# Optimization experiments

Hardware: AMD Instinct MI355X
Metric: run time of the kernel (lower is better)

The kernel has to match this reference:

```python
import jax, jax.numpy as jnp
import numpy as np

B, T, D = 4, 2048, 1024
HEADS = 8
D_K = D // HEADS


def setup_inputs() -> dict:
    key = jax.random.key(0)
    kq, kk, kv = jax.random.split(key, 3)
    return {
        "query": jax.random.normal(kq, (B, T, D), dtype=jnp.float32),
        "key": jax.random.normal(kk, (B, T, D), dtype=jnp.float32),
        "value": jax.random.normal(kv, (B, T, D), dtype=jnp.float32),
    }


def reference(query, key, value):
    b, t, d = query.shape
    # [B,T,D] -> [B,H,T,d_k]
    q = query.reshape(b, t, HEADS, D_K).transpose(0, 2, 1, 3)
    k = key.reshape(b, t, HEADS, D_K).transpose(0, 2, 1, 3)
    v = value.reshape(b, t, HEADS, D_K).transpose(0, 2, 1, 3)
    scale = 1.0 / jnp.sqrt(jnp.asarray(D_K, dtype=q.dtype))
    scores = jnp.einsum("bhqd,bhkd->bhqk", q, k) * scale  # [B,H,T,T]
    p_attn = jax.nn.softmax(scores, axis=-1)
    # sharpening: second softmax over 1000*p, clamp to [0,1]
    attn = jnp.clip(jax.nn.softmax(1000.0 * p_attn, axis=-1), 0.0, 1.0)
    x = jnp.einsum("bhqk,bhkd->bhqd", attn, v)  # [B,H,T,d_k]
    out = x.transpose(0, 2, 1, 3).reshape(b, t, HEADS * D_K)
    return out
```

## Files before the change

### kernel.cpp

```cpp
#include <hip/hip_runtime.h>


typedef __attribute__((ext_vector_type(4))) float f32x4;
typedef __attribute__((ext_vector_type(16))) float f32x16;
typedef __attribute__((ext_vector_type(8))) _Float16 h16x8;
typedef __attribute__((ext_vector_type(4))) _Float16 h16x4;
typedef __attribute__((ext_vector_type(8))) short s16x8;
typedef __attribute__((ext_vector_type(4))) short s16x4;
typedef __attribute__((ext_vector_type(2))) unsigned int u32x2;
typedef __attribute__((ext_vector_type(4))) unsigned int u32x4;

#define NB 4
#define T_ 2048
#define D_ 1024
#define NH 8
#define DK 128
#define BQ 64
#define NWG (NB * NH * (T_ / BQ))
#define KB2 32
#define NKC2 (T_ / KB2)
#define SCALE 0.08838834764831845f
#define SC2   0.12751741689839996f
#define MOFF2 11.541560327111707f
#define L2E   1.4426950408889634f

__device__ __forceinline__ unsigned int pk2(float a, float b) {
  return __builtin_bit_cast(unsigned int, __builtin_amdgcn_cvt_pkrtz(a, b));
}
#define H8(p) __builtin_bit_cast(h16x8, *(const s16x8*)(p))

__device__ __forceinline__ void gload16(const unsigned short* g, unsigned short* l) {
  __builtin_amdgcn_global_load_lds(
      (const __attribute__((address_space(1))) void*)g,
      (__attribute__((address_space(3))) void*)l, 16, 0, 0);
}

__global__ __launch_bounds__(256) void cvtK16(const float* __restrict__ Kg,
                                              unsigned short* __restrict__ K16) {
  const int t = threadIdx.x;
#pragma unroll
  for (int i = 0; i < 4; ++i) {
    const unsigned gid = blockIdx.x * 1024u + i * 256u + t;
    const unsigned bhk = gid >> 4, dg = gid & 15u;
    const unsigned b = bhk >> 14, rem = bhk & 16383u;
    const unsigned h = rem >> 11, k = rem & 2047u;
    const float* s = Kg + ((size_t)b * T_ + k) * D_ + h * DK + dg * 8;
    f32x4 x0 = *(const f32x4*)s, x1 = *(const f32x4*)(s + 4);
    h16x8 hv;
#pragma unroll
    for (int j = 0; j < 4; ++j) { hv[j] = (_Float16)x0[j]; hv[j + 4] = (_Float16)x1[j]; }
    *(u32x4*)(K16 + (size_t)gid * 8) = __builtin_bit_cast(u32x4, hv);
  }
}

__global__ __launch_bounds__(256) void trV16(const float* __restrict__ Vg,
                                             unsigned short* __restrict__ V16t) {
  __shared__ float vt[64][129];
  const int t = threadIdx.x;
  const int bh = blockIdx.x >> 5;
  const int kc = blockIdx.x & 31;
  const int b = bh >> 3, h = bh & 7;
  const float* src = Vg + ((size_t)b * T_ + kc * 64) * D_ + h * DK;
#pragma unroll
  for (int p = 0; p < 8; ++p) {
    const int j = t + p * 256;
    const int row = j >> 5, c4 = j & 31;
    f32x4 v = *(const f32x4*)(src + (size_t)row * D_ + c4 * 4);
#pragma unroll
    for (int i = 0; i < 4; ++i) vt[row][c4 * 4 + i] = v[i];
  }
  __syncthreads();
  unsigned short* dst = V16t + (size_t)bh * DK * T_ + (size_t)kc * 64;
#pragma unroll
  for (int i = 0; i < 4; ++i) {
    const int gg = t + i * 256;
    const int d = gg >> 3, kg = gg & 7;
    u32x4 pv;
#pragma unroll
    for (int jj = 0; jj < 4; ++jj)
      pv[jj] = pk2(vt[kg * 8 + 2 * jj][d], vt[kg * 8 + 2 * jj + 1][d]);
    *(u32x4*)(dst + (size_t)d * T_ + kg * 8) = pv;
  }
}

__global__ __launch_bounds__(128, 2) void simattn_v8(
    const float* __restrict__ Qg, const unsigned short* __restrict__ K16,
    const unsigned short* __restrict__ V16t, float* __restrict__ Og) {
  __shared__ __align__(16) unsigned short kf[2][KB2 * DK];
  __shared__ __align__(16) unsigned short vts[2][DK * KB2];

  const int tid  = threadIdx.x;
  const int wid2 = tid >> 6;
  const int lane = tid & 63;
  const int c    = lane & 31;
  const int g    = lane >> 5;
  const bool hi  = (g != 0);

  const int blk  = (blockIdx.x & 7) * (NWG >> 3) + (blockIdx.x >> 3);
  const int qblk = blk & (T_ / BQ - 1);
  const int h    = (blk >> 5) & (NH - 1);
  const int b    = blk >> 8;
  const int q0   = qblk * BQ;
  const size_t bh  = (size_t)b * (T_ * D_) + (size_t)h * DK;
  const int    bhp = b * NH + h;
  const unsigned short* kp16 = K16 + (size_t)bhp * (T_ * DK);
  const unsigned short* vp16 = V16t + (size_t)bhp * (DK * T_);

  h16x8 qf[8];
  {
    const float* qp = Qg + bh + (size_t)(q0 + wid2 * 32 + c) * D_;
#pragma unroll
    for (int step = 0; step < 8; ++step) {
      const int d0 = step * 16 + g * 8;
      f32x4 x0 = *(const f32x4*)(qp + d0);
      f32x4 x1 = *(const f32x4*)(qp + d0 + 4);
#pragma unroll
      for (int i = 0; i < 4; ++i) {
        qf[step][i]     = (_Float16)x0[i];
        qf[step][i + 4] = (_Float16)x1[i];
      }
    }
  }

  int koffs[4], voffs[4], ldst[4];
#pragma unroll
  for (int i = 0; i < 4; ++i) {
    const int id = wid2 * 4 + i;
    ldst[i] = id * 512 + lane * 8;
    {
      const int r = id * 4 + (lane >> 4), t = lane & 15;
      const int sk = 4 * ((id >> 1) & 1);
      koffs[i] = r * DK + ((((t - sk) & 15) ^ (r & 7)) * 8);
    }
    {
      const int d = id * 16 + (lane >> 2), t = lane & 3;
      voffs[i] = d * T_ + ((t ^ ((d >> 1) & 3)) * 8);
    }
  }
  auto stK = [&](int kc, int buf) {
    const unsigned short* s0 = kp16 + (size_t)kc * (KB2 * DK);
#pragma unroll
    for (int i = 0; i < 4; ++i) gload16(s0 + koffs[i], &kf[buf][ldst[i]]);
  };
  auto stV = [&](int kc, int buf) {
    const unsigned short* s0 = vp16 + kc * KB2;
#pragma unroll
    for (int i = 0; i < 4; ++i) gload16(s0 + voffs[i], &vts[buf][ldst[i]]);
  };

  int kread[8];
  {
    const int xr = c & 7, skr = 4 * ((c >> 3) & 1);
#pragma unroll
    for (int step = 0; step < 8; ++step)
      kread[step] = c * DK + (((((2 * step + g) ^ xr) + skr) & 15) * 8);
  }
  const int vsw = (c >> 1) & 3;

  auto qkT = [&](int buf) {
    f32x16 st;
#pragma unroll
    for (int i = 0; i < 16; ++i) st[i] = 0.f;
#pragma unroll
    for (int step = 0; step < 8; ++step) {
      st = __builtin_amdgcn_mfma_f32_32x32x16_f16(H8(&kf[buf][kread[step]]),
                                                  qf[step], st, 0, 0, 0);
    }
    return st;
  };

  float msc = -3.0e38f, l8 = 0.f;
  stK(0, 0);
  __syncthreads();
  for (int kc = 0; kc < NKC2; ++kc) {
    if (kc + 1 < NKC2) stK(kc + 1, (kc + 1) & 1);
    f32x16 st = qkT(kc & 1);
    float e[16];
#pragma unroll
    for (int r = 0; r < 16; ++r) {
      msc = fmaxf(msc, st[r]);
      e[r] = __builtin_amdgcn_exp2f(fmaf(st[r], SC2, -MOFF2));
    }
    float s0 = 0.f, s1 = 0.f, s2 = 0.f, s3 = 0.f;
#pragma unroll
    for (int r = 0; r < 4; ++r) {
      s0 += e[r]; s1 += e[4 + r]; s2 += e[8 + r]; s3 += e[12 + r];
    }
    l8 += (s0 + s1) + (s2 + s3);
    __syncthreads();
  }
  msc = fmaxf(msc, __shfl_xor(msc, 32));
  l8 += __shfl_xor(l8, 32);
  const float pm   = __builtin_amdgcn_exp2f(fmaf(msc, SC2, -MOFF2));
  const float ul2  = (1000.0f / l8) * L2E;
  const float mcu2 = -ul2 * pm;

  f32x16 y[4];
#pragma unroll
  for (int dt = 0; dt < 4; ++dt)
#pragma unroll
    for (int i = 0; i < 16; ++i) y[dt][i] = 0.f;
  float Wl = 0.f;

  stK(0, 0);
  stV(0, 0);
  __syncthreads();
  for (int kc = 0; kc < NKC2; ++kc) {
    if (kc + 1 < NKC2) { stK(kc + 1, (kc + 1) & 1); stV(kc + 1, (kc + 1) & 1); }
    const int buf = kc & 1;
    f32x16 st = qkT(buf);

    unsigned pw[8];
#pragma unroll
    for (int m = 0; m < 8; ++m) {
      const float p0 = __builtin_amdgcn_exp2f(fmaf(st[2 * m], SC2, -MOFF2));
      const float p1 = __builtin_amdgcn_exp2f(fmaf(st[2 * m + 1], SC2, -MOFF2));
      const float w0 = __builtin_amdgcn_exp2f(fmaf(p0, ul2, mcu2));
      const float w1 = __builtin_amdgcn_exp2f(fmaf(p1, ul2, mcu2));
      Wl += w0 + w1;
      pw[m] = pk2(w0, w1);
    }

#pragma unroll
    for (int hh = 0; hh < 2; ++hh) {
      const unsigned t0 = hi ? pw[4 * hh] : pw[4 * hh + 2];
      const unsigned t1 = hi ? pw[4 * hh + 1] : pw[4 * hh + 3];
      const unsigned r0 = (unsigned)__shfl_xor((int)t0, 32);
      const unsigned r1 = (unsigned)__shfl_xor((int)t1, 32);
      u32x4 aw;
      aw[0] = hi ? r0 : pw[4 * hh];
      aw[1] = hi ? r1 : pw[4 * hh + 1];
      aw[2] = hi ? pw[4 * hh + 2] : r0;
      aw[3] = hi ? pw[4 * hh + 3] : r1;
      const h16x8 af = __builtin_bit_cast(h16x8, aw);
#pragma unroll
      for (int dt = 0; dt < 4; ++dt) {
        const int d = dt * 32 + c;
        const h16x8 vf = H8(&vts[buf][d * KB2 + (((2 * hh + g) ^ vsw) * 8)]);
        y[dt] = __builtin_amdgcn_mfma_f32_32x32x16_f16(af, vf, y[dt], 0, 0, 0);
      }
    }
    __syncthreads();
  }

  Wl += __shfl_xor(Wl, 32);
  const float winv = 1.0f / Wl;

  float* ob = Og + bh + (size_t)(q0 + wid2 * 32) * D_;
#pragma unroll
  for (int r = 0; r < 16; ++r) {
    const int qrow = (r & 3) + 8 * (r >> 2) + 4 * g;
    const float wv = __shfl(winv, qrow);
#pragma unroll
    for (int dt = 0; dt < 4; ++dt) {
      ob[(size_t)qrow * D_ + dt * 32 + c] = y[dt][r] * wv;
    }
  }
}

__global__ __launch_bounds__(256, 4) void simattn_fb(
    const float* __restrict__ Qg, const float* __restrict__ Kg,
    const float* __restrict__ Vg, float* __restrict__ Og) {
  __shared__ __align__(16) unsigned short kfb[64][DK];
  __shared__ __align__(16) unsigned short vtb[DK][64];
  __shared__ __align__(16) unsigned int   wlb[4][16][32];

  const int tid  = threadIdx.x;
  const int wid  = tid >> 6;
  const int lane = tid & 63;
  const int lr   = lane & 15;
  const int lg   = lane >> 4;

  const int blk  = blockIdx.x;
  const int qblk = blk & (T_ / BQ - 1);
  const int h    = (blk >> 5) & (NH - 1);
  const int b    = blk >> 8;
  const int q0   = qblk * BQ;
  const size_t bh = (size_t)b * (T_ * D_) + (size_t)h * DK;

  h16x8 qf[4];
  {
    const float* qp = Qg + bh + (size_t)(q0 + wid * 16 + lr) * D_;
#pragma unroll
    for (int s = 0; s < 4; ++s) {
      const int d0 = s * 32 + lg * 8;
      f32x4 x0 = *(const f32x4*)(qp + d0);
      f32x4 x1 = *(const f32x4*)(qp + d0 + 4);
#pragma unroll
      for (int i = 0; i < 4; ++i) { qf[s][i] = (_Float16)x0[i]; qf[s][i+4] = (_Float16)x1[i]; }
    }
  }
  auto stageK = [&](int kc) {
    const float* kp = Kg + bh + (size_t)kc * 64 * D_;
#pragma unroll
    for (int p = 0; p < 8; ++p) {
      const int j = tid + p * 256;
      const int row = j >> 5, c4 = j & 31;
      f32x4 v = *(const f32x4*)(kp + (size_t)row * D_ + c4 * 4);
      h16x4 hv;
#pragma unroll
      for (int i = 0; i < 4; ++i) hv[i] = (_Float16)v[i];
      const int e = (c4 * 4) ^ ((row & 7) << 3);
      *(s16x4*)&kfb[row][e] = __builtin_bit_cast(s16x4, hv);
    }
  };
  auto qkT = [&](f32x4* st) {
#pragma unroll
    for (int nt = 0; nt < 4; ++nt) st[nt] = (f32x4){0.f, 0.f, 0.f, 0.f};
#pragma unroll
    for (int s = 0; s < 4; ++s) {
#pragma unroll
      for (int nt = 0; nt < 4; ++nt) {
        const int kr = nt * 16 + lr;
        const int e = (s * 32 + lg * 8) ^ ((kr & 7) << 3);
        st[nt] = __builtin_amdgcn_mfma_f32_16x16x32_f16(H8(&kfb[kr][e]), qf[s], st[nt], 0, 0, 0);
      }
    }
  };
  float msc = -3.0e38f, l8 = 0.f;
  for (int kc = 0; kc < 32; ++kc) {
    __syncthreads();
    stageK(kc);
    __syncthreads();
    f32x4 st[4];
    qkT(st);
#pragma unroll
    for (int nt = 0; nt < 4; ++nt)
#pragma unroll
      for (int r = 0; r < 4; ++r) {
        const float s = st[nt][r];
        msc = fmaxf(msc, s);
        l8 += __builtin_amdgcn_exp2f(fmaf(s, SC2, -MOFF2));
      }
  }
  msc = fmaxf(msc, __shfl_xor(msc, 16));
  msc = fmaxf(msc, __shfl_xor(msc, 32));
  l8 += __shfl_xor(l8, 16);
  l8 += __shfl_xor(l8, 32);
  const float pm   = __builtin_amdgcn_exp2f(fmaf(msc, SC2, -MOFF2));
  const float ul2  = (1000.0f / l8) * L2E;
  const float mcu2 = -ul2 * pm;

  f32x4 y[8];
#pragma unroll
  for (int dt = 0; dt < 8; ++dt) y[dt] = (f32x4){0.f, 0.f, 0.f, 0.f};
  float Wl = 0.f;
  const int dv  = tid & 127;
  const int kg0 = tid >> 7;
  for (int kc = 0; kc < 32; ++kc) {
    __syncthreads();
    stageK(kc);
    {
      const float* vp = Vg + bh + (size_t)kc * 64 * D_ + dv;
#pragma unroll
      for (int i = 0; i < 4; ++i) {
        const int kg = kg0 + 2 * i;
        const float* vq = vp + (size_t)kg * 8 * D_;
        u32x4 pv;
        pv[0] = pk2(vq[0], vq[D_]);
        pv[1] = pk2(vq[2 * D_], vq[3 * D_]);
        pv[2] = pk2(vq[4 * D_], vq[5 * D_]);
        pv[3] = pk2(vq[6 * D_], vq[7 * D_]);
        *(u32x4*)&vtb[dv][(kg ^ (dv & 7)) * 8] = pv;
      }
    }
    __syncthreads();
    f32x4 st[4];
    qkT(st);
#pragma unroll
    for (int nt = 0; nt < 4; ++nt) {
      float w[4];
#pragma unroll
      for (int r = 0; r < 4; ++r) {
        const float pp = __builtin_amdgcn_exp2f(fmaf(st[nt][r], SC2, -MOFF2));
        w[r] = __builtin_amdgcn_exp2f(fmaf(pp, ul2, mcu2));
      }
      Wl += (w[0] + w[1]) + (w[2] + w[3]);
      u32x2 pk;
      pk[0] = pk2(w[0], w[1]);
      pk[1] = pk2(w[2], w[3]);
      *(u32x2*)&wlb[wid][lr][(nt * 8 + lg * 2) ^ ((lr & 7) << 2)] = pk;
    }
#pragma unroll
    for (int ks = 0; ks < 2; ++ks) {
      h16x8 af = H8((const unsigned short*)&wlb[wid][lr][(ks * 16 + lg * 4) ^ ((lr & 7) << 2)]);
#pragma unroll
      for (int dt = 0; dt < 8; ++dt) {
        const int d = dt * 16 + lr;
        h16x8 vf = H8(&vtb[d][((ks * 4 + lg) ^ (d & 7)) * 8]);
        y[dt] = __builtin_amdgcn_mfma_f32_16x16x32_f16(af, vf, y[dt], 0, 0, 0);
      }
    }
  }
  Wl += __shfl_xor(Wl, 16);
  Wl += __shfl_xor(Wl, 32);
  const float winv = 1.0f / Wl;
  float* op = Og + bh + (size_t)(q0 + wid * 16) * D_;
#pragma unroll
  for (int r = 0; r < 4; ++r) {
    const float wv = __shfl(winv, lg * 4 + r);
#pragma unroll
    for (int dt = 0; dt < 8; ++dt)
      op[(size_t)(lg * 4 + r) * D_ + dt * 16 + lr] = y[dt][r] * wv;
  }
}

extern "C" void kernel_launch(void* const* d_in, const int* in_sizes, int n_in,
                              void* d_out, int out_size, void* d_ws, size_t ws_size,
                              hipStream_t stream) {
  (void)in_sizes; (void)n_in; (void)out_size;
  const float* Q = (const float*)d_in[0];
  const float* K = (const float*)d_in[1];
  const float* V = (const float*)d_in[2];
  float* O = (float*)d_out;
  const size_t half = (size_t)NB * NH * T_ * DK * 2;
  if (ws_size >= 2 * half) {
    unsigned short* K16  = (unsigned short*)d_ws;
    unsigned short* V16t = (unsigned short*)((char*)d_ws + half);
    cvtK16<<<dim3(1024), 256, 0, stream>>>(K, K16);
    trV16<<<dim3(1024), 256, 0, stream>>>(V, V16t);
    simattn_v8<<<dim3(NWG), 128, 0, stream>>>(Q, K16, V16t, O);
  } else {
    simattn_fb<<<dim3(NWG), 256, 0, stream>>>(Q, K, V, O);
  }
}
```

Baseline: 173.1 us.

## Pre-swizzle K/V into MFMA fragment layout and load directly to registers

Merges the K conversion and V transpose into one prep kernel that writes fp16 K and V in the exact per-lane MFMA fragment order. The attention kernel becomes one wave per 32-query tile and reads fragments straight from global memory into registers with coalesced 16-byte loads. This drops the LDS staging, double buffering and block barriers. In exchange it gives up K/V reuse across waves within a block and relies on L2 and outstanding loads to hide global latency.

```diff
diff --git a/kernel.cpp b/kernel.cpp
--- a/kernel.cpp
+++ b/kernel.cpp
@@ -15,10 +15,8 @@
 #define D_ 1024
 #define NH 8
 #define DK 128
-#define BQ 64
-#define NWG (NB * NH * (T_ / BQ))
-#define KB2 32
-#define NKC2 (T_ / KB2)
+#define NKC9 64
+#define NWG9 (NB * NH * (T_ / 32))
 #define SCALE 0.08838834764831845f
 #define SC2   0.12751741689839996f
 #define MOFF2 11.541560327111707f
@@ -29,86 +27,67 @@
 }
 #define H8(p) __builtin_bit_cast(h16x8, *(const s16x8*)(p))
 
-__device__ __forceinline__ void gload16(const unsigned short* g, unsigned short* l) {
-  __builtin_amdgcn_global_load_lds(
-      (const __attribute__((address_space(1))) void*)g,
-      (__attribute__((address_space(3))) void*)l, 16, 0, 0);
-}
-
-__global__ __launch_bounds__(256) void cvtK16(const float* __restrict__ Kg,
-                                              unsigned short* __restrict__ K16) {
-  const int t = threadIdx.x;
+__global__ __launch_bounds__(256) void prep9(const float* __restrict__ Kg,
+                                             const float* __restrict__ Vg,
+                                             unsigned short* __restrict__ Kf,
+                                             unsigned short* __restrict__ Vf) {
+  __shared__ unsigned short klds[32][136];
+  __shared__ unsigned short vlds[32][136];
+  const int t   = threadIdx.x;
+  const int bid = blockIdx.x;
+  const int bh = bid >> 6, kc = bid & 63;
+  const int b = bh >> 3, h = bh & 7;
+  const float* ks = Kg + ((size_t)b * T_ + kc * 32) * D_ + h * DK;
+  const float* vs = Vg + ((size_t)b * T_ + kc * 32) * D_ + h * DK;
 #pragma unroll
   for (int i = 0; i < 4; ++i) {
-    const unsigned gid = blockIdx.x * 1024u + i * 256u + t;
-    const unsigned bhk = gid >> 4, dg = gid & 15u;
-    const unsigned b = bhk >> 14, rem = bhk & 16383u;
-    const unsigned h = rem >> 11, k = rem & 2047u;
-    const float* s = Kg + ((size_t)b * T_ + k) * D_ + h * DK + dg * 8;
-    f32x4 x0 = *(const f32x4*)s, x1 = *(const f32x4*)(s + 4);
-    h16x8 hv;
-#pragma unroll
-    for (int j = 0; j < 4; ++j) { hv[j] = (_Float16)x0[j]; hv[j + 4] = (_Float16)x1[j]; }
-    *(u32x4*)(K16 + (size_t)gid * 8) = __builtin_bit_cast(u32x4, hv);
-  }
-}
-
-__global__ __launch_bounds__(256) void trV16(const float* __restrict__ Vg,
-                                             unsigned short* __restrict__ V16t) {
-  __shared__ float vt[64][129];
-  const int t = threadIdx.x;
-  const int bh = blockIdx.x >> 5;
-  const int kc = blockIdx.x & 31;
-  const int b = bh >> 3, h = bh & 7;
-  const float* src = Vg + ((size_t)b * T_ + kc * 64) * D_ + h * DK;
-#pragma unroll
-  for (int p = 0; p < 8; ++p) {
-    const int j = t + p * 256;
-    const int row = j >> 5, c4 = j & 31;
-    f32x4 v = *(const f32x4*)(src + (size_t)row * D_ + c4 * 4);
-#pragma unroll
-    for (int i = 0; i < 4; ++i) vt[row][c4 * 4 + i] = v[i];
+    const int gidx = i * 256 + t;
+    const int row = gidx >> 5, c4 = gidx & 31;
+    f32x4 kv = *(const f32x4*)(ks + (size_t)row * D_ + c4 * 4);
+    f32x4 vv = *(const f32x4*)(vs + (size_t)row * D_ + c4 * 4);
+    h16x4 kh, vh;
+#pragma unroll
+    for (int j = 0; j < 4; ++j) { kh[j] = (_Float16)kv[j]; vh[j] = (_Float16)vv[j]; }
+    *(s16x4*)&klds[row][c4 * 4] = __builtin_bit_cast(s16x4, kh);
+    *(s16x4*)&vlds[row][c4 * 4] = __builtin_bit_cast(s16x4, vh);
   }
   __syncthreads();
-  unsigned short* dst = V16t + (size_t)bh * DK * T_ + (size_t)kc * 64;
-#pragma unroll
-  for (int i = 0; i < 4; ++i) {
-    const int gg = t + i * 256;
-    const int d = gg >> 3, kg = gg & 7;
-    u32x4 pv;
-#pragma unroll
-    for (int jj = 0; jj < 4; ++jj)
-      pv[jj] = pk2(vt[kg * 8 + 2 * jj][d], vt[kg * 8 + 2 * jj + 1][d]);
-    *(u32x4*)(dst + (size_t)d * T_ + kg * 8) = pv;
-  }
-}
-
-__global__ __launch_bounds__(128, 2) void simattn_v8(
-    const float* __restrict__ Qg, const unsigned short* __restrict__ K16,
-    const unsigned short* __restrict__ V16t, float* __restrict__ Og) {
-  __shared__ __align__(16) unsigned short kf[2][KB2 * DK];
-  __shared__ __align__(16) unsigned short vts[2][DK * KB2];
-
-  const int tid  = threadIdx.x;
-  const int wid2 = tid >> 6;
-  const int lane = tid & 63;
-  const int c    = lane & 31;
-  const int g    = lane >> 5;
-  const bool hi  = (g != 0);
-
-  const int blk  = (blockIdx.x & 7) * (NWG >> 3) + (blockIdx.x >> 3);
-  const int qblk = blk & (T_ / BQ - 1);
-  const int h    = (blk >> 5) & (NH - 1);
-  const int b    = blk >> 8;
-  const int q0   = qblk * BQ;
-  const size_t bh  = (size_t)b * (T_ * D_) + (size_t)h * DK;
-  const int    bhp = b * NH + h;
-  const unsigned short* kp16 = K16 + (size_t)bhp * (T_ * DK);
-  const unsigned short* vp16 = V16t + (size_t)bhp * (DK * T_);
+  unsigned short* kd = Kf + ((size_t)bh * 64 + kc) * 4096;
+  unsigned short* vd = Vf + ((size_t)bh * 64 + kc) * 4096;
+#pragma unroll
+  for (int i = 0; i < 2; ++i) {
+    const int gr = i * 256 + t;
+    const int sl = gr >> 6, l = gr & 63;
+    const int gg = l >> 5, cc = l & 31;
+    *(s16x8*)(kd + gr * 8) = *(const s16x8*)&klds[cc][sl * 16 + gg * 8];
+    const int hh = sl >> 2, dt = sl & 3;
+    s16x8 tv;
+#pragma unroll
+    for (int j = 0; j < 8; ++j)
+      tv[j] = (short)vlds[hh * 16 + gg * 8 + j][dt * 32 + cc];
+    *(s16x8*)(vd + gr * 8) = tv;
+  }
+}
+
+__global__ __launch_bounds__(64, 2) void simattn_v9(
+    const float* __restrict__ Qg, const unsigned short* __restrict__ Kf,
+    const unsigned short* __restrict__ Vf, float* __restrict__ Og) {
+  const int lane = threadIdx.x;
+  const int c = lane & 31, g = lane >> 5;
+  const bool hi = (g != 0);
+
+  const int bid = blockIdx.x;
+  const int blk = (bid & 7) * (NWG9 >> 3) + (bid >> 3);
+  const int qt = blk & 63, h = (blk >> 6) & 7, b = blk >> 9;
+  const int q0 = qt * 32;
+  const size_t bhf = (size_t)b * (T_ * D_) + (size_t)h * DK;
+  const int bhp = b * NH + h;
+  const unsigned short* kb0 = Kf + (size_t)bhp * (64 * 4096) + lane * 8;
+  const unsigned short* vb0 = Vf + (size_t)bhp * (64 * 4096) + lane * 8;
 
   h16x8 qf[8];
   {
-    const float* qp = Qg + bh + (size_t)(q0 + wid2 * 32 + c) * D_;
+    const float* qp = Qg + bhf + (size_t)(q0 + c) * D_;
 #pragma unroll
     for (int step = 0; step < 8; ++step) {
       const int d0 = step * 16 + g * 8;
@@ -122,59 +101,20 @@
     }
   }
 
-  int koffs[4], voffs[4], ldst[4];
-#pragma unroll
-  for (int i = 0; i < 4; ++i) {
-    const int id = wid2 * 4 + i;
-    ldst[i] = id * 512 + lane * 8;
-    {
-      const int r = id * 4 + (lane >> 4), t = lane & 15;
-      const int sk = 4 * ((id >> 1) & 1);
-      koffs[i] = r * DK + ((((t - sk) & 15) ^ (r & 7)) * 8);
-    }
-    {
-      const int d = id * 16 + (lane >> 2), t = lane & 3;
-      voffs[i] = d * T_ + ((t ^ ((d >> 1) & 3)) * 8);
-    }
-  }
-  auto stK = [&](int kc, int buf) {
-    const unsigned short* s0 = kp16 + (size_t)kc * (KB2 * DK);
-#pragma unroll
-    for (int i = 0; i < 4; ++i) gload16(s0 + koffs[i], &kf[buf][ldst[i]]);
-  };
-  auto stV = [&](int kc, int buf) {
-    const unsigned short* s0 = vp16 + kc * KB2;
-#pragma unroll
-    for (int i = 0; i < 4; ++i) gload16(s0 + voffs[i], &vts[buf][ldst[i]]);
-  };
-
-  int kread[8];
-  {
-    const int xr = c & 7, skr = 4 * ((c >> 3) & 1);
-#pragma unroll
-    for (int step = 0; step < 8; ++step)
-      kread[step] = c * DK + (((((2 * step + g) ^ xr) + skr) & 15) * 8);
-  }
-  const int vsw = (c >> 1) & 3;
-
-  auto qkT = [&](int buf) {
+  float msc = -3.0e38f, l8 = 0.f;
+#pragma unroll 2
+  for (int kc = 0; kc < NKC9; ++kc) {
+    const unsigned short* kp = kb0 + kc * 4096;
+    s16x8 kb[8];
+#pragma unroll
+    for (int s = 0; s < 8; ++s) kb[s] = *(const s16x8*)(kp + s * 512);
     f32x16 st;
 #pragma unroll
     for (int i = 0; i < 16; ++i) st[i] = 0.f;
 #pragma unroll
-    for (int step = 0; step < 8; ++step) {
-      st = __builtin_amdgcn_mfma_f32_32x32x16_f16(H8(&kf[buf][kread[step]]),
-                                                  qf[step], st, 0, 0, 0);
-    }
-    return st;
-  };
-
-  float msc = -3.0e38f, l8 = 0.f;
-  stK(0, 0);
-  __syncthreads();
-  for (int kc = 0; kc < NKC2; ++kc) {
-    if (kc + 1 < NKC2) stK(kc + 1, (kc + 1) & 1);
-    f32x16 st = qkT(kc & 1);
+    for (int s = 0; s < 8; ++s)
+      st = __builtin_amdgcn_mfma_f32_32x32x16_f16(__builtin_bit_cast(h16x8, kb[s]),
+                                                  qf[s], st, 0, 0, 0);
     float e[16];
 #pragma unroll
     for (int r = 0; r < 16; ++r) {
@@ -187,7 +127,6 @@
       s0 += e[r]; s1 += e[4 + r]; s2 += e[8 + r]; s3 += e[12 + r];
     }
     l8 += (s0 + s1) + (s2 + s3);
-    __syncthreads();
   }
   msc = fmaxf(msc, __shfl_xor(msc, 32));
   l8 += __shfl_xor(l8, 32);
@@ -202,13 +141,21 @@
     for (int i = 0; i < 16; ++i) y[dt][i] = 0.f;
   float Wl = 0.f;
 
-  stK(0, 0);
-  stV(0, 0);
-  __syncthreads();
-  for (int kc = 0; kc < NKC2; ++kc) {
-    if (kc + 1 < NKC2) { stK(kc + 1, (kc + 1) & 1); stV(kc + 1, (kc + 1) & 1); }
-    const int buf = kc & 1;
-    f32x16 st = qkT(buf);
+  for (int kc = 0; kc < NKC9; ++kc) {
+    const unsigned short* kp = kb0 + kc * 4096;
+    const unsigned short* vp = vb0 + kc * 4096;
+    s16x8 kb[8], vb[8];
+#pragma unroll
+    for (int s = 0; s < 8; ++s) kb[s] = *(const s16x8*)(kp + s * 512);
+#pragma unroll
+    for (int s = 0; s < 8; ++s) vb[s] = *(const s16x8*)(vp + s * 512);
+    f32x16 st;
+#pragma unroll
+    for (int i = 0; i < 16; ++i) st[i] = 0.f;
+#pragma unroll
+    for (int s = 0; s < 8; ++s)
+      st = __builtin_amdgcn_mfma_f32_32x32x16_f16(__builtin_bit_cast(h16x8, kb[s]),
+                                                  qf[s], st, 0, 0, 0);
 
     unsigned pw[8];
 #pragma unroll
@@ -235,18 +182,16 @@
       const h16x8 af = __builtin_bit_cast(h16x8, aw);
 #pragma unroll
       for (int dt = 0; dt < 4; ++dt) {
-        const int d = dt * 32 + c;
-        const h16x8 vf = H8(&vts[buf][d * KB2 + (((2 * hh + g) ^ vsw) * 8)]);
-        y[dt] = __builtin_amdgcn_mfma_f32_32x32x16_f16(af, vf, y[dt], 0, 0, 0);
-      }
-    }
-    __syncthreads();
+        y[dt] = __builtin_amdgcn_mfma_f32_32x32x16_f16(
+            af, __builtin_bit_cast(h16x8, vb[hh * 4 + dt]), y[dt], 0, 0, 0);
+      }
+    }
   }
 
   Wl += __shfl_xor(Wl, 32);
   const float winv = 1.0f / Wl;
 
-  float* ob = Og + bh + (size_t)(q0 + wid2 * 32) * D_;
+  float* ob = Og + bhf + (size_t)q0 * D_;
 #pragma unroll
   for (int r = 0; r < 16; ++r) {
     const int qrow = (r & 3) + 8 * (r >> 2) + 4 * g;
@@ -272,10 +217,10 @@
   const int lg   = lane >> 4;
 
   const int blk  = blockIdx.x;
-  const int qblk = blk & (T_ / BQ - 1);
+  const int qblk = blk & 31;
   const int h    = (blk >> 5) & (NH - 1);
   const int b    = blk >> 8;
-  const int q0   = qblk * BQ;
+  const int q0   = qblk * 64;
   const size_t bh = (size_t)b * (T_ * D_) + (size_t)h * DK;
 
   h16x8 qf[4];
@@ -415,12 +360,11 @@
   float* O = (float*)d_out;
   const size_t half = (size_t)NB * NH * T_ * DK * 2;
   if (ws_size >= 2 * half) {
-    unsigned short* K16  = (unsigned short*)d_ws;
-    unsigned short* V16t = (unsigned short*)((char*)d_ws + half);
-    cvtK16<<<dim3(1024), 256, 0, stream>>>(K, K16);
-    trV16<<<dim3(1024), 256, 0, stream>>>(V, V16t);
-    simattn_v8<<<dim3(NWG), 128, 0, stream>>>(Q, K16, V16t, O);
+    unsigned short* Kf = (unsigned short*)d_ws;
+    unsigned short* Vf = (unsigned short*)((char*)d_ws + half);
+    prep9<<<dim3(2048), 256, 0, stream>>>(K, V, Kf, Vf);
+    simattn_v9<<<dim3(NWG9), 64, 0, stream>>>(Q, Kf, Vf, O);
   } else {
-    simattn_fb<<<dim3(NWG), 256, 0, stream>>>(Q, K, V, O);
-  }
-}
+    simattn_fb<<<dim3(NB * NH * (T_ / 64)), 256, 0, stream>>>(Q, K, V, O);
+  }
+}
```

Measured after the change: 181.1 us. +4.6%, slower.
